# Optimization experiments

Measured on AMD Instinct MI355X. Metric: run time of the kernel, lower is better.

## Reference

```python
import jax, jax.numpy as jnp
import numpy as np

D_MODEL = 640
KW = 32                                  # kernel_width -> content_kernel (compression (1,1))
SUPER = np.array([5, 5, 2, 1, 1])        # supersampling per subhead
DIL = np.array([1, 1, 2, 4, 8])          # dilation rate per subhead
SUBHEADS = 5
HEADS = int(SUPER.sum())                 # 14
DH = D_MODEL // SUBHEADS                 # 128
B, N = 2, 1024
KC = KW                                  # content kernel width
DIL_PER_HEAD = np.repeat(DIL, SUPER)     # dilation used by each of the 14 value heads


def _windows(seq, bias, dil):
    """Banded (dilated, stride-1, 'same'-padded) windows of a projected sequence.

    seq: (B, N, DH). The original zero-pads the raw sequence, then applies the
    per-head Linear; projecting a zero vector yields the bias, so padding the
    projected sequence with `bias` is mathematically identical.
    Returns (B, N, KC, DH) with out[b, l, j] = padded[b, l + j*dil].
    """
    dil = int(dil)
    pad_total = (KC - 1) * dil           # effective kernel minus 1, stride 1 -> same length
    pl = pad_total // 2
    pr = pad_total - pl
    b = seq.shape[0]
    left = jnp.broadcast_to(bias, (b, pl, DH))
    right = jnp.broadcast_to(bias, (b, pr, DH))
    padded = jnp.concatenate([left, seq, right], axis=1)
    idx = jnp.arange(N)[:, None] + jnp.arange(KC)[None, :] * dil  # (N, KC)
    return padded[:, idx]


def setup_inputs() -> dict:
    key = jax.random.key(0)
    ks = jax.random.split(key, 13)
    f = lambda k, sh, s=1.0: jax.random.normal(k, sh, dtype=jnp.float32) * s
    return {
        "query": f(ks[0], (B, N, D_MODEL)),
        "key": f(ks[1], (B, N, D_MODEL)),
        "value": f(ks[2], (B, N, D_MODEL)),
        "Qk": f(ks[3], (SUBHEADS, DH, D_MODEL), 0.04),
        "Qb": f(ks[4], (SUBHEADS, DH), 0.02),
        "Kk": f(ks[5], (SUBHEADS, DH, D_MODEL), 0.04),
        "Kb": f(ks[6], (SUBHEADS, DH), 0.02),
        "Vk": f(ks[7], (HEADS, DH, D_MODEL), 0.04),
        "Vb": f(ks[8], (HEADS, DH), 0.02),
        "Sk": f(ks[9], (HEADS, KC, KC), 0.1),   # Pos_Sampling kernel, Kq=1 so in=out=KC
        "Sb": f(ks[10], (HEADS, KC), 0.02),
        "Ck": f(ks[11], (D_MODEL, HEADS * DH), 0.02),  # Collapse kernel
        "Cb": f(ks[12], (D_MODEL,), 0.0),
    }


def reference(query, key, value, Qk, Qb, Kk, Kb, Vk, Vb, Sk, Sb, Ck, Cb):
    # Per-subhead Q/K projections (query_kernel=1, stride=1 -> one query per position)
    q = jnp.einsum('bnd,sod->bnso', query, Qk) + Qb          # (B,N,5,DH)
    kproj = jnp.einsum('bnd,sod->bnso', key, Kk) + Kb        # (B,N,5,DH)
    kwin = jnp.stack(
        [_windows(kproj[:, :, s], Kb[s], DIL[s]) for s in range(SUBHEADS)],
        axis=2)                                              # (B,N,5,KC,DH)
    # Banded scores (original applies no 1/sqrt(d) scaling)
    score = jnp.einsum('bnsd,bnskd->bnsk', q, kwin)          # (B,N,5,KC)
    # Supersample subhead scores into heads, then learned positional resampling
    score = jnp.repeat(score, SUPER, axis=2, total_repeat_length=HEADS)  # (B,N,14,KC)
    score = jnp.einsum('bnhk,hjk->bnhj', score, Sk) + Sb     # Pos_Sampling Linear
    w = jax.nn.softmax(score, axis=-1)
    # Per-head value projection; each head windows with its subhead's dilation
    vproj = jnp.einsum('bnd,hod->bnho', value, Vk) + Vb      # (B,N,14,DH)
    vwin = jnp.stack(
        [_windows(vproj[:, :, h], Vb[h], DIL_PER_HEAD[h]) for h in range(HEADS)],
        axis=2)                                              # (B,N,14,KC,DH)
    attn = jnp.einsum('bnhk,bnhkd->bnhd', w, vwin)           # (B,N,14,DH)
    flat = attn.reshape(attn.shape[0], attn.shape[1], HEADS * DH)
    return jnp.einsum('bnf,of->bno', flat, Ck) + Cb          # (B,N,D_MODEL)
```

## Files before the change

### kernel.cpp

```cpp
#include <hip/hip_runtime.h>
#include <hip/hip_bf16.h>

using bf16 = __hip_bfloat16;
typedef __attribute__((ext_vector_type(8))) short s16x8;
typedef __attribute__((ext_vector_type(4))) float f32x4;
typedef unsigned int u32;

__device__ __forceinline__ float b2f(short u) {
    union { float f; u32 i; } x; x.i = ((u32)(unsigned short)u) << 16; return x.f;
}
__device__ __forceinline__ short f2b(float f) {
    bf16 h = (bf16)f; return *(short*)&h;
}

__device__ __forceinline__ void glds16(const bf16* g, bf16* l) {
#if __has_builtin(__builtin_amdgcn_global_load_lds)
    __builtin_amdgcn_global_load_lds(
        (const __attribute__((address_space(1))) u32*)g,
        (__attribute__((address_space(3))) u32*)l, 16, 0, 0);
#else
    *(uint4*)l = *(const uint4*)g;
#endif
}

struct CvtArgs { const float* src[13]; bf16* dst[13]; int n[13]; int bb[14]; };
__global__ __launch_bounds__(256)
void convert_kernel(CvtArgs a) {
    const int blk = blockIdx.x;
    int s = 0;
    while (s < 12 && blk >= a.bb[s + 1]) ++s;
    const int base = (blk - a.bb[s]) * 1024 + threadIdx.x * 4;
    if (base >= a.n[s]) return;
    float4 v = *(const float4*)(a.src[s] + base);
    ushort4 o;
    o.x = (unsigned short)f2b(v.x); o.y = (unsigned short)f2b(v.y);
    o.z = (unsigned short)f2b(v.z); o.w = (unsigned short)f2b(v.w);
    *(ushort4*)(a.dst[s] + base) = o;
}

template<int BM, int BN, bool OUT_F32>
__device__ __forceinline__ void gemm_core(
    const bf16* __restrict__ A, const bf16* __restrict__ W,
    const bf16* __restrict__ bias, void* __restrict__ out,
    int m0, int n0, int N, int K, bf16* lA, bf16* lB) {
    constexpr int WM = BM / 2, WN = BN / 2, FM = WM / 16, FN = WN / 16;
    constexpr int SA = BM / 64, SB = BN / 64;
    const int tid = threadIdx.x;
    const int wave = tid >> 6, lane = tid & 63;
    const int wr = wave >> 1, wc = wave & 1;
    const int quad = lane >> 4, lm = lane & 15;
    f32x4 acc[FM][FN] = {};
    for (int k0 = 0; k0 < K; k0 += 32) {
#pragma unroll
        for (int q = 0; q < SA; ++q) {
            int sl = q * 256 + tid;
            glds16(A + (size_t)(m0 + (sl >> 2)) * K + k0 + (sl & 3) * 8, lA + sl * 8);
        }
#pragma unroll
        for (int q = 0; q < SB; ++q) {
            int sl = q * 256 + tid;
            glds16(W + (size_t)(n0 + (sl >> 2)) * K + k0 + (sl & 3) * 8, lB + sl * 8);
        }
        __syncthreads();
        s16x8 af[FM], bf_[FN];
#pragma unroll
        for (int i = 0; i < FM; ++i)
            af[i] = *(const s16x8*)&lA[(wr * WM + i * 16 + lm) * 32 + quad * 8];
#pragma unroll
        for (int j = 0; j < FN; ++j)
            bf_[j] = *(const s16x8*)&lB[(wc * WN + j * 16 + lm) * 32 + quad * 8];
#pragma unroll
        for (int i = 0; i < FM; ++i)
#pragma unroll
            for (int j = 0; j < FN; ++j)
                acc[i][j] = __builtin_amdgcn_mfma_f32_16x16x32_bf16(af[i], bf_[j], acc[i][j], 0, 0, 0);
        __syncthreads();
    }
#pragma unroll
    for (int i = 0; i < FM; ++i) {
        const int rbase = m0 + wr * WM + i * 16 + quad * 4;
#pragma unroll
        for (int j = 0; j < FN; ++j) {
            const int col = n0 + wc * WN + j * 16 + lm;
            const float bv = (float)bias[col];
#pragma unroll
            for (int r = 0; r < 4; ++r) {
                float v = acc[i][j][r] + bv;
                size_t off = (size_t)(rbase + r) * N + col;
                if (OUT_F32) ((float*)out)[off] = v;
                else         ((bf16*)out)[off] = (bf16)v;
            }
        }
    }
}

__global__ __launch_bounds__(256)
void proj_kernel(const bf16* __restrict__ qc, const bf16* __restrict__ kc,
                 const bf16* __restrict__ vc,
                 const bf16* __restrict__ Qkc, const bf16* __restrict__ Kkc,
                 const bf16* __restrict__ Vkc,
                 const bf16* __restrict__ Qbc, const bf16* __restrict__ Kbc,
                 const bf16* __restrict__ Vbc,
                 float* __restrict__ qp, float* __restrict__ kp,
                 bf16* __restrict__ vp) {
    __shared__ __align__(16) bf16 lA[128 * 32];
    __shared__ __align__(16) bf16 lB[128 * 32];
    const int L = blockIdx.x, xcd = L & 7, i = L >> 3;
    const int m0 = (xcd * 2 + i / 24) * 128;
    const int nid = i % 24;
    if (nid < 5)
        gemm_core<128, 128, true >(qc, Qkc, Qbc, qp, m0, nid * 128, 640, 640, lA, lB);
    else if (nid < 10)
        gemm_core<128, 128, true >(kc, Kkc, Kbc, kp, m0, (nid - 5) * 128, 640, 640, lA, lB);
    else
        gemm_core<128, 128, false>(vc, Vkc, Vbc, vp, m0, (nid - 10) * 128, 1792, 640, lA, lB);
}

__global__ __launch_bounds__(256)
void collapse_kernel(const bf16* __restrict__ atn, const bf16* __restrict__ Ckc,
                     const bf16* __restrict__ Cbc, float* __restrict__ out) {
    __shared__ __align__(16) bf16 lA[128 * 32];
    __shared__ __align__(16) bf16 lB[64 * 32];
    const int L = blockIdx.x, xcd = L & 7, i = L >> 3;
    const int m0 = (xcd * 2 + i / 10) * 128;
    const int n0 = (i % 10) * 64;
    gemm_core<128, 64, true>(atn, Ckc, Cbc, out, m0, n0, 640, 1792, lA, lB);
}

__global__ __launch_bounds__(256)
void attn_v4(const float* __restrict__ qp, const float* __restrict__ kp,
             const bf16* __restrict__ vp,
             const bf16* __restrict__ Kbc, const bf16* __restrict__ Vbc,
             const bf16* __restrict__ Skc, const bf16* __restrict__ Sbc,
             bf16* __restrict__ atn) {
    const int pos = ((blockIdx.x & 7) << 8) | (blockIdx.x >> 3);
    const int b = pos >> 10, l = pos & 1023;
    const int t = threadIdx.x;
    __shared__ float qs[640];
    __shared__ float sc5[5 * 32];
    __shared__ float sc14[14 * 32];
    __shared__ float w14T[32 * 14];

    if (t < 160) ((float4*)qs)[t] = ((const float4*)(qp + (size_t)pos * 640))[t];
    __syncthreads();

    {
        const int j = t >> 3, p = t & 7;
#pragma unroll
        for (int s = 0; s < 5; ++s) {
            const int dil = (s < 2) ? 1 : (1 << (s - 1));
            const int pl = (31 * dil) >> 1;
            const int row = l + j * dil - pl;
            const float* q = qs + s * 128 + p * 4;
            float acc = 0.f;
            if (row >= 0 && row < 1024) {
                const float* kr = kp + (size_t)((b << 10) | row) * 640 + s * 128 + p * 4;
#pragma unroll
                for (int g = 0; g < 4; ++g) {
                    float4 kv = *(const float4*)(kr + g * 32);
                    float4 qv = *(const float4*)(q + g * 32);
                    acc += qv.x * kv.x + qv.y * kv.y + qv.z * kv.z + qv.w * kv.w;
                }
            } else {
                const bf16* kb = Kbc + s * 128 + p * 4;
#pragma unroll
                for (int g = 0; g < 4; ++g) {
                    float4 qv = *(const float4*)(q + g * 32);
                    acc += qv.x * (float)kb[g * 32] + qv.y * (float)kb[g * 32 + 1]
                         + qv.z * (float)kb[g * 32 + 2] + qv.w * (float)kb[g * 32 + 3];
                }
            }
            acc += __shfl_xor(acc, 1);
            acc += __shfl_xor(acc, 2);
            acc += __shfl_xor(acc, 4);
            if (p == 0) sc5[s * 32 + j] = acc;
        }
    }
    __syncthreads();

    for (int idx = t; idx < 448; idx += 256) {
        const int h = idx >> 5;
        const int s = (h < 5) ? 0 : (h < 10) ? 1 : (h < 12) ? 2 : (h == 12) ? 3 : 4;
        const s16x8* sk = (const s16x8*)((const short*)Skc + idx * 32);
        const float* sc = sc5 + s * 32;
        float acc = b2f(((const short*)Sbc)[idx]);
#pragma unroll
        for (int g = 0; g < 4; ++g) {
            s16x8 kk = sk[g];
#pragma unroll
            for (int r = 0; r < 8; ++r) acc += sc[g * 8 + r] * b2f(kk[r]);
        }
        sc14[idx] = acc;
    }
    __syncthreads();

    if (t < 224) {
        const int h = t >> 4, u = t & 15;
        float s0 = sc14[h * 32 + u], s1 = sc14[h * 32 + u + 16];
        float mx = fmaxf(s0, s1);
#pragma unroll
        for (int m = 1; m < 16; m <<= 1) mx = fmaxf(mx, __shfl_xor(mx, m));
        float e0 = __expf(s0 - mx), e1 = __expf(s1 - mx);
        float sum = e0 + e1;
#pragma unroll
        for (int m = 1; m < 16; m <<= 1) sum += __shfl_xor(sum, m);
        float inv = 1.f / sum;
        w14T[u * 14 + h] = e0 * inv;
        w14T[(u + 16) * 14 + h] = e1 * inv;
    }
    __syncthreads();

    if (t < 224) {
        const int h = t >> 4, d8 = (t & 15) * 8;
        const int dil = (h < 10) ? 1 : (h < 12) ? 2 : (h == 12) ? 4 : 8;
        const int pl = (31 * dil) >> 1;
        const int col = h * 128 + d8;
        float acc[8] = {};
#pragma unroll
        for (int j = 0; j < 32; ++j) {
            const int row = l + j * dil - pl;
            const short* src = (row >= 0 && row < 1024)
                ? (const short*)vp + (size_t)((b << 10) | row) * 1792 + col
                : (const short*)Vbc + col;
            s16x8 v8 = *(const s16x8*)src;
            const float w = w14T[j * 14 + h];
#pragma unroll
            for (int r = 0; r < 8; ++r) acc[r] += w * b2f(v8[r]);
        }
        union { uint4 u; short h16[8]; } o;
#pragma unroll
        for (int r = 0; r < 8; ++r) o.h16[r] = f2b(acc[r]);
        *(uint4*)((short*)atn + (size_t)pos * 1792 + col) = o.u;
    }
}

extern "C" void kernel_launch(void* const* d_in, const int* in_sizes, int n_in,
                              void* d_out, int out_size, void* d_ws, size_t ws_size,
                              hipStream_t stream) {
    const int M = 2048;
    char* w = (char*)d_ws;
    size_t off = 0;
    auto alloc = [&](size_t bytes) -> char* {
        off = (off + 255) & ~(size_t)255;
        char* p = w + off; off += bytes; return p;
    };
    bf16* qc  = (bf16*)alloc(1310720 * 2);
    bf16* kc  = (bf16*)alloc(1310720 * 2);
    bf16* vc  = (bf16*)alloc(1310720 * 2);
    bf16* Qkc = (bf16*)alloc(409600 * 2);
    bf16* Qbc = (bf16*)alloc(640 * 2);
    bf16* Kkc = (bf16*)alloc(409600 * 2);
    bf16* Kbc = (bf16*)alloc(640 * 2);
    bf16* Vkc = (bf16*)alloc(1146880 * 2);
    bf16* Vbc = (bf16*)alloc(1792 * 2);
    bf16* Skc = (bf16*)alloc(14336 * 2);
    bf16* Sbc = (bf16*)alloc(448 * 2);
    bf16* Ckc = (bf16*)alloc(1146880 * 2);
    bf16* Cbc = (bf16*)alloc(640 * 2);
    float* qp = (float*)alloc((size_t)M * 640 * 4);
    float* kp = (float*)alloc((size_t)M * 640 * 4);
    bf16*  vp = (bf16*)alloc((size_t)M * 1792 * 2);
    bf16*  atn = (bf16*)alloc((size_t)M * 1792 * 2);

    CvtArgs ca;
    bf16* dsts[13] = {qc, kc, vc, Qkc, Qbc, Kkc, Kbc, Vkc, Vbc, Skc, Sbc, Ckc, Cbc};
    const int ns[13] = {1310720, 1310720, 1310720, 409600, 640, 409600, 640,
                        1146880, 1792, 14336, 448, 1146880, 640};
    int cum = 0;
    for (int i = 0; i < 13; ++i) {
        ca.src[i] = (const float*)d_in[i];
        ca.dst[i] = dsts[i];
        ca.n[i] = ns[i];
        ca.bb[i] = cum;
        cum += (ns[i] + 1023) / 1024;
    }
    ca.bb[13] = cum;

    dim3 blk(256);
    convert_kernel<<<dim3(cum), blk, 0, stream>>>(ca);
    proj_kernel<<<dim3(384), blk, 0, stream>>>(qc, kc, vc, Qkc, Kkc, Vkc,
                                               Qbc, Kbc, Vbc, qp, kp, vp);
    attn_v4<<<dim3(2048), blk, 0, stream>>>(qp, kp, vp, Kbc, Vbc, Skc, Sbc, atn);
    collapse_kernel<<<dim3(160), blk, 0, stream>>>(atn, Ckc, Cbc, (float*)d_out);
}
```

Before: 171.6 us.

## Fuse activation fp32->bf16 conversion into GEMM loads and register-prefetch tiles

The projection GEMM now reads fp32 activations directly and converts them to bf16 while loading, so the three activation tensors no longer pass through the separate convert kernel and a bf16 round trip in memory. The GEMM loop switches from direct global-to-LDS loads to register double buffering: the next k-tile is fetched into registers while MFMAs run on the current LDS tile. Tile sizes shrink (proj 128x64, collapse 64x64) to double the block counts for better CU occupancy. The cost is more register use, fp32 activation reads inside the GEMM, and lost reuse from the smaller tiles.

```diff
diff --git a/kernel.cpp b/kernel.cpp
--- a/kernel.cpp
+++ b/kernel.cpp
@@ -13,22 +13,12 @@
     bf16 h = (bf16)f; return *(short*)&h;
 }
 
-__device__ __forceinline__ void glds16(const bf16* g, bf16* l) {
-#if __has_builtin(__builtin_amdgcn_global_load_lds)
-    __builtin_amdgcn_global_load_lds(
-        (const __attribute__((address_space(1))) u32*)g,
-        (__attribute__((address_space(3))) u32*)l, 16, 0, 0);
-#else
-    *(uint4*)l = *(const uint4*)g;
-#endif
-}
-
-struct CvtArgs { const float* src[13]; bf16* dst[13]; int n[13]; int bb[14]; };
+struct CvtArgs { const float* src[10]; bf16* dst[10]; int n[10]; int bb[11]; };
 __global__ __launch_bounds__(256)
 void convert_kernel(CvtArgs a) {
     const int blk = blockIdx.x;
     int s = 0;
-    while (s < 12 && blk >= a.bb[s + 1]) ++s;
+    while (s < 9 && blk >= a.bb[s + 1]) ++s;
     const int base = (blk - a.bb[s]) * 1024 + threadIdx.x * 4;
     if (base >= a.n[s]) return;
     float4 v = *(const float4*)(a.src[s] + base);
@@ -38,9 +28,9 @@
     *(ushort4*)(a.dst[s] + base) = o;
 }
 
-template<int BM, int BN, bool OUT_F32>
-__device__ __forceinline__ void gemm_core(
-    const bf16* __restrict__ A, const bf16* __restrict__ W,
+template<int BM, int BN, bool A_F32, bool OUT_F32>
+__device__ __forceinline__ void gemm_pipe(
+    const void* __restrict__ A, const bf16* __restrict__ W,
     const bf16* __restrict__ bias, void* __restrict__ out,
     int m0, int n0, int N, int K, bf16* lA, bf16* lB) {
     constexpr int WM = BM / 2, WN = BN / 2, FM = WM / 16, FN = WN / 16;
@@ -49,19 +39,42 @@
     const int wave = tid >> 6, lane = tid & 63;
     const int wr = wave >> 1, wc = wave & 1;
     const int quad = lane >> 4, lm = lane & 15;
+    uint4 ra[SA], rb[SB];
+
+    auto loadA = [&](int k0) {
+#pragma unroll
+        for (int q = 0; q < SA; ++q) {
+            const int sl = q * 256 + tid, row = sl >> 2, col = (sl & 3) * 8;
+            if (A_F32) {
+                const float* g = (const float*)A + (size_t)(m0 + row) * K + k0 + col;
+                float4 f0 = *(const float4*)g;
+                float4 f1 = *(const float4*)(g + 4);
+                union { uint4 u; short h[8]; } p;
+                p.h[0] = f2b(f0.x); p.h[1] = f2b(f0.y); p.h[2] = f2b(f0.z); p.h[3] = f2b(f0.w);
+                p.h[4] = f2b(f1.x); p.h[5] = f2b(f1.y); p.h[6] = f2b(f1.z); p.h[7] = f2b(f1.w);
+                ra[q] = p.u;
+            } else {
+                ra[q] = *(const uint4*)((const bf16*)A + (size_t)(m0 + row) * K + k0 + col);
+            }
+        }
+    };
+    auto loadB = [&](int k0) {
+#pragma unroll
+        for (int q = 0; q < SB; ++q) {
+            const int sl = q * 256 + tid, row = sl >> 2, col = (sl & 3) * 8;
+            rb[q] = *(const uint4*)(W + (size_t)(n0 + row) * K + k0 + col);
+        }
+    };
+
     f32x4 acc[FM][FN] = {};
+    loadA(0); loadB(0);
     for (int k0 = 0; k0 < K; k0 += 32) {
 #pragma unroll
-        for (int q = 0; q < SA; ++q) {
-            int sl = q * 256 + tid;
-            glds16(A + (size_t)(m0 + (sl >> 2)) * K + k0 + (sl & 3) * 8, lA + sl * 8);
-        }
-#pragma unroll
-        for (int q = 0; q < SB; ++q) {
-            int sl = q * 256 + tid;
-            glds16(W + (size_t)(n0 + (sl >> 2)) * K + k0 + (sl & 3) * 8, lB + sl * 8);
-        }
+        for (int q = 0; q < SA; ++q) *(uint4*)(lA + (q * 256 + tid) * 8) = ra[q];
+#pragma unroll
+        for (int q = 0; q < SB; ++q) *(uint4*)(lB + (q * 256 + tid) * 8) = rb[q];
         __syncthreads();
+        if (k0 + 32 < K) { loadA(k0 + 32); loadB(k0 + 32); }
         s16x8 af[FM], bf_[FN];
 #pragma unroll
         for (int i = 0; i < FM; ++i)
@@ -95,8 +108,8 @@
 }
 
 __global__ __launch_bounds__(256)
-void proj_kernel(const bf16* __restrict__ qc, const bf16* __restrict__ kc,
-                 const bf16* __restrict__ vc,
+void proj_kernel(const float* __restrict__ q, const float* __restrict__ k,
+                 const float* __restrict__ v,
                  const bf16* __restrict__ Qkc, const bf16* __restrict__ Kkc,
                  const bf16* __restrict__ Vkc,
                  const bf16* __restrict__ Qbc, const bf16* __restrict__ Kbc,
@@ -104,27 +117,27 @@
                  float* __restrict__ qp, float* __restrict__ kp,
                  bf16* __restrict__ vp) {
     __shared__ __align__(16) bf16 lA[128 * 32];
-    __shared__ __align__(16) bf16 lB[128 * 32];
+    __shared__ __align__(16) bf16 lB[64 * 32];
     const int L = blockIdx.x, xcd = L & 7, i = L >> 3;
-    const int m0 = (xcd * 2 + i / 24) * 128;
-    const int nid = i % 24;
-    if (nid < 5)
-        gemm_core<128, 128, true >(qc, Qkc, Qbc, qp, m0, nid * 128, 640, 640, lA, lB);
-    else if (nid < 10)
-        gemm_core<128, 128, true >(kc, Kkc, Kbc, kp, m0, (nid - 5) * 128, 640, 640, lA, lB);
+    const int m0 = (xcd * 2 + i / 48) * 128;
+    const int nid = i % 48;
+    if (nid < 10)
+        gemm_pipe<128, 64, true, true >(q, Qkc, Qbc, qp, m0, nid * 64, 640, 640, lA, lB);
+    else if (nid < 20)
+        gemm_pipe<128, 64, true, true >(k, Kkc, Kbc, kp, m0, (nid - 10) * 64, 640, 640, lA, lB);
     else
-        gemm_core<128, 128, false>(vc, Vkc, Vbc, vp, m0, (nid - 10) * 128, 1792, 640, lA, lB);
+        gemm_pipe<128, 64, true, false>(v, Vkc, Vbc, vp, m0, (nid - 20) * 64, 1792, 640, lA, lB);
 }
 
 __global__ __launch_bounds__(256)
 void collapse_kernel(const bf16* __restrict__ atn, const bf16* __restrict__ Ckc,
                      const bf16* __restrict__ Cbc, float* __restrict__ out) {
-    __shared__ __align__(16) bf16 lA[128 * 32];
+    __shared__ __align__(16) bf16 lA[64 * 32];
     __shared__ __align__(16) bf16 lB[64 * 32];
     const int L = blockIdx.x, xcd = L & 7, i = L >> 3;
-    const int m0 = (xcd * 2 + i / 10) * 128;
+    const int m0 = (xcd * 4 + i / 10) * 64;
     const int n0 = (i % 10) * 64;
-    gemm_core<128, 64, true>(atn, Ckc, Cbc, out, m0, n0, 640, 1792, lA, lB);
+    gemm_pipe<64, 64, false, true>(atn, Ckc, Cbc, out, m0, n0, 640, 1792, lA, lB);
 }
 
 __global__ __launch_bounds__(256)
@@ -244,9 +257,6 @@
         off = (off + 255) & ~(size_t)255;
         char* p = w + off; off += bytes; return p;
     };
-    bf16* qc  = (bf16*)alloc(1310720 * 2);
-    bf16* kc  = (bf16*)alloc(1310720 * 2);
-    bf16* vc  = (bf16*)alloc(1310720 * 2);
     bf16* Qkc = (bf16*)alloc(409600 * 2);
     bf16* Qbc = (bf16*)alloc(640 * 2);
     bf16* Kkc = (bf16*)alloc(409600 * 2);
@@ -263,23 +273,23 @@
     bf16*  atn = (bf16*)alloc((size_t)M * 1792 * 2);
 
     CvtArgs ca;
-    bf16* dsts[13] = {qc, kc, vc, Qkc, Qbc, Kkc, Kbc, Vkc, Vbc, Skc, Sbc, Ckc, Cbc};
-    const int ns[13] = {1310720, 1310720, 1310720, 409600, 640, 409600, 640,
-                        1146880, 1792, 14336, 448, 1146880, 640};
+    bf16* dsts[10] = {Qkc, Qbc, Kkc, Kbc, Vkc, Vbc, Skc, Sbc, Ckc, Cbc};
+    const int ns[10] = {409600, 640, 409600, 640, 1146880, 1792, 14336, 448, 1146880, 640};
     int cum = 0;
-    for (int i = 0; i < 13; ++i) {
-        ca.src[i] = (const float*)d_in[i];
+    for (int i = 0; i < 10; ++i) {
+        ca.src[i] = (const float*)d_in[3 + i];
         ca.dst[i] = dsts[i];
         ca.n[i] = ns[i];
         ca.bb[i] = cum;
         cum += (ns[i] + 1023) / 1024;
     }
-    ca.bb[13] = cum;
+    ca.bb[10] = cum;
 
     dim3 blk(256);
     convert_kernel<<<dim3(cum), blk, 0, stream>>>(ca);
-    proj_kernel<<<dim3(384), blk, 0, stream>>>(qc, kc, vc, Qkc, Kkc, Vkc,
-                                               Qbc, Kbc, Vbc, qp, kp, vp);
+    proj_kernel<<<dim3(768), blk, 0, stream>>>(
+        (const float*)d_in[0], (const float*)d_in[1], (const float*)d_in[2],
+        Qkc, Kkc, Vkc, Qbc, Kbc, Vbc, qp, kp, vp);
     attn_v4<<<dim3(2048), blk, 0, stream>>>(qp, kp, vp, Kbc, Vbc, Skc, Sbc, atn);
-    collapse_kernel<<<dim3(160), blk, 0, stream>>>(atn, Ckc, Cbc, (float*)d_out);
-}
+    collapse_kernel<<<dim3(320), blk, 0, stream>>>(atn, Ckc, Cbc, (float*)d_out);
+}
```

New measurement: 165.6 us (median of 3 runs). -3.5%, faster.

## Register-prefetch GEMM tiles and shrink tiles to raise block counts

Applied to the files above, without the earlier changes.

Replaces the direct global-to-LDS loads in the projection and collapse GEMMs with register-staged prefetching, so the next K-slice is loaded while MFMAs run on the current one. Projection tiles shrink from 128x128 to 128x64, which doubles the grid to 768 blocks. Collapse becomes a dedicated 64x64 kernel with a K-step of 64 and padded LDS rows to avoid bank conflicts, which doubles its grid to 320 blocks. The cost is more register use and smaller per-block reuse.

```diff
diff --git a/kernel.cpp b/kernel.cpp
--- a/kernel.cpp
+++ b/kernel.cpp
@@ -11,16 +11,6 @@
 }
 __device__ __forceinline__ short f2b(float f) {
     bf16 h = (bf16)f; return *(short*)&h;
-}
-
-__device__ __forceinline__ void glds16(const bf16* g, bf16* l) {
-#if __has_builtin(__builtin_amdgcn_global_load_lds)
-    __builtin_amdgcn_global_load_lds(
-        (const __attribute__((address_space(1))) u32*)g,
-        (__attribute__((address_space(3))) u32*)l, 16, 0, 0);
-#else
-    *(uint4*)l = *(const uint4*)g;
-#endif
 }
 
 struct CvtArgs { const float* src[13]; bf16* dst[13]; int n[13]; int bb[14]; };
@@ -38,50 +28,54 @@
     *(ushort4*)(a.dst[s] + base) = o;
 }
 
-template<int BM, int BN, bool OUT_F32>
-__device__ __forceinline__ void gemm_core(
+template<bool OUT_F32>
+__device__ __forceinline__ void gemm_128x64(
     const bf16* __restrict__ A, const bf16* __restrict__ W,
     const bf16* __restrict__ bias, void* __restrict__ out,
     int m0, int n0, int N, int K, bf16* lA, bf16* lB) {
-    constexpr int WM = BM / 2, WN = BN / 2, FM = WM / 16, FN = WN / 16;
-    constexpr int SA = BM / 64, SB = BN / 64;
     const int tid = threadIdx.x;
     const int wave = tid >> 6, lane = tid & 63;
     const int wr = wave >> 1, wc = wave & 1;
     const int quad = lane >> 4, lm = lane & 15;
-    f32x4 acc[FM][FN] = {};
+    uint4 ra[2], rb;
+    auto loadA = [&](int k0) {
+#pragma unroll
+        for (int q = 0; q < 2; ++q) {
+            const int sl = q * 256 + tid;
+            ra[q] = *(const uint4*)(A + (size_t)(m0 + (sl >> 2)) * K + k0 + (sl & 3) * 8);
+        }
+    };
+    auto loadB = [&](int k0) {
+        rb = *(const uint4*)(W + (size_t)(n0 + (tid >> 2)) * K + k0 + (tid & 3) * 8);
+    };
+    f32x4 acc[4][2] = {};
+    loadA(0); loadB(0);
     for (int k0 = 0; k0 < K; k0 += 32) {
 #pragma unroll
-        for (int q = 0; q < SA; ++q) {
-            int sl = q * 256 + tid;
-            glds16(A + (size_t)(m0 + (sl >> 2)) * K + k0 + (sl & 3) * 8, lA + sl * 8);
-        }
-#pragma unroll
-        for (int q = 0; q < SB; ++q) {
-            int sl = q * 256 + tid;
-            glds16(W + (size_t)(n0 + (sl >> 2)) * K + k0 + (sl & 3) * 8, lB + sl * 8);
-        }
+        for (int q = 0; q < 2; ++q) *(uint4*)(lA + (q * 256 + tid) * 8) = ra[q];
+        *(uint4*)(lB + tid * 8) = rb;
         __syncthreads();
-        s16x8 af[FM], bf_[FN];
-#pragma unroll
-        for (int i = 0; i < FM; ++i)
-            af[i] = *(const s16x8*)&lA[(wr * WM + i * 16 + lm) * 32 + quad * 8];
-#pragma unroll
-        for (int j = 0; j < FN; ++j)
-            bf_[j] = *(const s16x8*)&lB[(wc * WN + j * 16 + lm) * 32 + quad * 8];
-#pragma unroll
-        for (int i = 0; i < FM; ++i)
-#pragma unroll
-            for (int j = 0; j < FN; ++j)
+        if (k0 + 32 < K) { loadA(k0 + 32); loadB(k0 + 32); }
+        s16x8 af[4], bf_[2];
+#pragma unroll
+        for (int i = 0; i < 4; ++i)
+            af[i] = *(const s16x8*)&lA[(wr * 64 + i * 16 + lm) * 32 + quad * 8];
+#pragma unroll
+        for (int j = 0; j < 2; ++j)
+            bf_[j] = *(const s16x8*)&lB[(wc * 32 + j * 16 + lm) * 32 + quad * 8];
+#pragma unroll
+        for (int i = 0; i < 4; ++i)
+#pragma unroll
+            for (int j = 0; j < 2; ++j)
                 acc[i][j] = __builtin_amdgcn_mfma_f32_16x16x32_bf16(af[i], bf_[j], acc[i][j], 0, 0, 0);
         __syncthreads();
     }
 #pragma unroll
-    for (int i = 0; i < FM; ++i) {
-        const int rbase = m0 + wr * WM + i * 16 + quad * 4;
-#pragma unroll
-        for (int j = 0; j < FN; ++j) {
-            const int col = n0 + wc * WN + j * 16 + lm;
+    for (int i = 0; i < 4; ++i) {
+        const int rbase = m0 + wr * 64 + i * 16 + quad * 4;
+#pragma unroll
+        for (int j = 0; j < 2; ++j) {
+            const int col = n0 + wc * 32 + j * 16 + lm;
             const float bv = (float)bias[col];
 #pragma unroll
             for (int r = 0; r < 4; ++r) {
@@ -104,27 +98,80 @@
                  float* __restrict__ qp, float* __restrict__ kp,
                  bf16* __restrict__ vp) {
     __shared__ __align__(16) bf16 lA[128 * 32];
-    __shared__ __align__(16) bf16 lB[128 * 32];
+    __shared__ __align__(16) bf16 lB[64 * 32];
     const int L = blockIdx.x, xcd = L & 7, i = L >> 3;
-    const int m0 = (xcd * 2 + i / 24) * 128;
-    const int nid = i % 24;
-    if (nid < 5)
-        gemm_core<128, 128, true >(qc, Qkc, Qbc, qp, m0, nid * 128, 640, 640, lA, lB);
-    else if (nid < 10)
-        gemm_core<128, 128, true >(kc, Kkc, Kbc, kp, m0, (nid - 5) * 128, 640, 640, lA, lB);
+    const int m0 = (xcd * 2 + i / 48) * 128;
+    const int nid = i % 48;
+    if (nid < 10)
+        gemm_128x64<true >(qc, Qkc, Qbc, qp, m0, nid * 64, 640, 640, lA, lB);
+    else if (nid < 20)
+        gemm_128x64<true >(kc, Kkc, Kbc, kp, m0, (nid - 10) * 64, 640, 640, lA, lB);
     else
-        gemm_core<128, 128, false>(vc, Vkc, Vbc, vp, m0, (nid - 10) * 128, 1792, 640, lA, lB);
+        gemm_128x64<false>(vc, Vkc, Vbc, vp, m0, (nid - 20) * 64, 1792, 640, lA, lB);
 }
 
 __global__ __launch_bounds__(256)
 void collapse_kernel(const bf16* __restrict__ atn, const bf16* __restrict__ Ckc,
                      const bf16* __restrict__ Cbc, float* __restrict__ out) {
-    __shared__ __align__(16) bf16 lA[128 * 32];
-    __shared__ __align__(16) bf16 lB[64 * 32];
+    __shared__ __align__(16) bf16 lA[64 * 72];
+    __shared__ __align__(16) bf16 lB[64 * 72];
     const int L = blockIdx.x, xcd = L & 7, i = L >> 3;
-    const int m0 = (xcd * 2 + i / 10) * 128;
+    const int m0 = (xcd * 4 + i / 10) * 64;
     const int n0 = (i % 10) * 64;
-    gemm_core<128, 64, true>(atn, Ckc, Cbc, out, m0, n0, 640, 1792, lA, lB);
+    const int K = 1792, N = 640;
+    const int tid = threadIdx.x;
+    const int wave = tid >> 6, lane = tid & 63;
+    const int wr = wave >> 1, wc = wave & 1;
+    const int quad = lane >> 4, lm = lane & 15;
+    uint4 ra[2], rb[2];
+    auto loadAB = [&](int k0) {
+#pragma unroll
+        for (int q = 0; q < 2; ++q) {
+            const int sl = q * 256 + tid, row = sl >> 3, col8 = (sl & 7) * 8;
+            ra[q] = *(const uint4*)(atn + (size_t)(m0 + row) * K + k0 + col8);
+            rb[q] = *(const uint4*)(Ckc + (size_t)(n0 + row) * K + k0 + col8);
+        }
+    };
+    f32x4 acc[2][2] = {};
+    loadAB(0);
+    for (int k0 = 0; k0 < K; k0 += 64) {
+#pragma unroll
+        for (int q = 0; q < 2; ++q) {
+            const int sl = q * 256 + tid, row = sl >> 3, col8 = (sl & 7) * 8;
+            *(uint4*)(lA + row * 72 + col8) = ra[q];
+            *(uint4*)(lB + row * 72 + col8) = rb[q];
+        }
+        __syncthreads();
+        if (k0 + 64 < K) loadAB(k0 + 64);
+#pragma unroll
+        for (int kk = 0; kk < 2; ++kk) {
+            s16x8 af[2], bf_[2];
+#pragma unroll
+            for (int i2 = 0; i2 < 2; ++i2)
+                af[i2] = *(const s16x8*)&lA[(wr * 32 + i2 * 16 + lm) * 72 + kk * 32 + quad * 8];
+#pragma unroll
+            for (int j = 0; j < 2; ++j)
+                bf_[j] = *(const s16x8*)&lB[(wc * 32 + j * 16 + lm) * 72 + kk * 32 + quad * 8];
+#pragma unroll
+            for (int i2 = 0; i2 < 2; ++i2)
+#pragma unroll
+                for (int j = 0; j < 2; ++j)
+                    acc[i2][j] = __builtin_amdgcn_mfma_f32_16x16x32_bf16(af[i2], bf_[j], acc[i2][j], 0, 0, 0);
+        }
+        __syncthreads();
+    }
+#pragma unroll
+    for (int i2 = 0; i2 < 2; ++i2) {
+        const int rbase = m0 + wr * 32 + i2 * 16 + quad * 4;
+#pragma unroll
+        for (int j = 0; j < 2; ++j) {
+            const int col = n0 + wc * 32 + j * 16 + lm;
+            const float bv = (float)Cbc[col];
+#pragma unroll
+            for (int r = 0; r < 4; ++r)
+                out[(size_t)(rbase + r) * N + col] = acc[i2][j][r] + bv;
+        }
+    }
 }
 
 __global__ __launch_bounds__(256)
@@ -278,8 +325,8 @@
 
     dim3 blk(256);
     convert_kernel<<<dim3(cum), blk, 0, stream>>>(ca);
-    proj_kernel<<<dim3(384), blk, 0, stream>>>(qc, kc, vc, Qkc, Kkc, Vkc,
+    proj_kernel<<<dim3(768), blk, 0, stream>>>(qc, kc, vc, Qkc, Kkc, Vkc,
                                                Qbc, Kbc, Vbc, qp, kp, vp);
     attn_v4<<<dim3(2048), blk, 0, stream>>>(qp, kp, vp, Kbc, Vbc, Skc, Sbc, atn);
-    collapse_kernel<<<dim3(160), blk, 0, stream>>>(atn, Ckc, Cbc, (float*)d_out);
-}
+    collapse_kernel<<<dim3(320), blk, 0, stream>>>(atn, Ckc, Cbc, (float*)d_out);
+}
```

New measurement: 237.3 us. 1.38x slower.
